# Kernel optimization log

Hardware: AMD Instinct MI355X
Metric: run time of the kernel (lower is better)

Reference implementation:

```python
import jax, jax.numpy as jnp
import numpy as np

D = 256
H = 4
DH = D // H
DFF = 1024
EPS = 1e-5


def _split_heads(x):
    B, L, _ = x.shape
    return x.reshape(B, L, H, DH).transpose(0, 2, 1, 3)  # [B,H,L,dh]


def _merge_heads(o):
    B, h, L, dh = o.shape
    return o.transpose(0, 2, 1, 3).reshape(B, L, h * dh)


def _attention(Q, K, V, M):
    # Q,K,V: [B,H,Lq/Lk,dh]; M: [B,Lq,Lk] or [B,1,Lk]
    A = jnp.einsum('bhqd,bhkd->bhqk', Q, K) / (DH ** 0.5)
    A = jnp.where(M[:, None] == 0, -jnp.inf, A)
    A = jax.nn.softmax(A, axis=-1)
    return jnp.einsum('bhqk,bhkd->bhqd', A, V)


def _layernorm(x, g, b):
    mu = jnp.mean(x, axis=-1, keepdims=True)
    var = jnp.mean(jnp.square(x - mu), axis=-1, keepdims=True)
    return (x - mu) * jax.lax.rsqrt(var + EPS) * g + b


def setup_inputs() -> dict:
    key = jax.random.key(0)
    ks = jax.random.split(key, 14)
    B, T, S = 16, 1024, 1024
    s = 1.0 / (D ** 0.5)
    inp = {
        'X_target': jax.random.normal(ks[0], (B, T, D), jnp.float32),
        'outputMask': jnp.ones((B, T), jnp.float32),
        'X_encoder': jax.random.normal(ks[1], (B, S, D), jnp.float32),
        'inputMask': jnp.ones((B, S), jnp.float32),
        'Wq1': jax.random.normal(ks[2], (D, D), jnp.float32) * s,
        'Wk1': jax.random.normal(ks[3], (D, D), jnp.float32) * s,
        'Wv1': jax.random.normal(ks[4], (D, D), jnp.float32) * s,
        'Wo1': jax.random.normal(ks[5], (D, D), jnp.float32) * s,
        'Wq2': jax.random.normal(ks[6], (D, D), jnp.float32) * s,
        'Wk2': jax.random.normal(ks[7], (D, D), jnp.float32) * s,
        'Wv2': jax.random.normal(ks[8], (D, D), jnp.float32) * s,
        'Wo2': jax.random.normal(ks[9], (D, D), jnp.float32) * s,
        'W1': jax.random.normal(ks[10], (DFF, D), jnp.float32) * s,
        'W2': jax.random.normal(ks[11], (D, DFF), jnp.float32) * (1.0 / (DFF ** 0.5)),
        'g1': jnp.ones((D,), jnp.float32), 'b1': jnp.zeros((D,), jnp.float32),
        'g2': jnp.ones((D,), jnp.float32), 'b2': jnp.zeros((D,), jnp.float32),
        'g3': jnp.ones((D,), jnp.float32), 'b3': jnp.zeros((D,), jnp.float32),
    }
    return inp


def reference(X_target, outputMask, X_encoder, inputMask,
              Wq1, Wk1, Wv1, Wo1, Wq2, Wk2, Wv2, Wo2,
              W1, W2, g1, b1, g2, b2, g3, b3):
    T = X_target.shape[1]
    # combined causal * padding mask (intended tril of ones)
    tril = jnp.tril(jnp.ones((T, T), X_target.dtype))
    M_self = outputMask[:, None, :] * tril  # [B,T,T]
    M_cross = inputMask[:, None, :]         # [B,1,S]

    # masked self-attention (Linear: x @ W.T)
    Q = _split_heads(X_target @ Wq1.T)
    K = _split_heads(X_target @ Wk1.T)
    V = _split_heads(X_target @ Wv1.T)
    O = _merge_heads(_attention(Q, K, V, M_self)) @ Wo1.T
    X = X_target + _layernorm(O, g1, b1)  # AddNorm (dropout eval=identity)

    # cross-attention; note: output proj is O @ Wo2 (no transpose) in source
    Q = _split_heads(X @ Wq2.T)
    K = _split_heads(X_encoder @ Wk2.T)
    V = _split_heads(X_encoder @ Wv2.T)
    O = _merge_heads(_attention(Q, K, V, M_cross)) @ Wo2
    X = X + _layernorm(O, g2, b2)

    # FFN with ReLU after both linears (as in source)
    F = jax.nn.relu(jax.nn.relu(X @ W1.T) @ W2.T)
    X = X + _layernorm(F, g3, b3)
    return X
```

## Files before the change

### kernel.cpp

```cpp
#include <hip/hip_runtime.h>
#include <math.h>

#define D_ 256
#define H_ 4
#define DH_ 64
#define NKT_ 16
#define TPB_BITS 10
#define SCL2E_ 0.18033688011112042f

typedef __attribute__((ext_vector_type(8))) short bf16x8;
typedef __attribute__((ext_vector_type(4))) short short4v;
typedef __attribute__((ext_vector_type(4))) float f32x4;

__device__ __forceinline__ short f2bf(float x) {
  union { float f; unsigned u; } c; c.f = x;
  unsigned r = (c.u + 0x7fffu + ((c.u >> 16) & 1u)) >> 16;
  return (short)r;
}
__device__ __forceinline__ float bf2f(short s) {
  union { unsigned u; float f; } c; c.u = ((unsigned)(unsigned short)s) << 16;
  return c.f;
}
__device__ __forceinline__ unsigned cvtpk(float lo, float hi) {
  unsigned r;
  asm("v_cvt_pk_bf16_f32 %0, %1, %2" : "=v"(r) : "v"(lo), "v"(hi));
  return r;
}
#if __has_builtin(__builtin_amdgcn_exp2f)
#define EXP2F(x) __builtin_amdgcn_exp2f(x)
#else
#define EXP2F(x) __expf(0.6931471805599453f * (x))
#endif

__device__ __forceinline__ void gl_lds16(const void* g, void* lds) {
  __builtin_amdgcn_global_load_lds((const __attribute__((address_space(1))) void*)g,
                                   (__attribute__((address_space(3))) void*)lds,
                                   16, 0, 0);
}

__global__ __launch_bounds__(256) void mask_bias(const float* __restrict__ m0,
                                                 const float* __restrict__ m1,
                                                 float* __restrict__ o0,
                                                 float* __restrict__ o1,
                                                 float* __restrict__ f0,
                                                 float* __restrict__ f1, int n) {
  int i = blockIdx.x * 256 + threadIdx.x;
  if (i < n) {
    o0[i] = (m0[i] != 0.f) ? 0.f : -1e30f;
    o1[i] = (m1[i] != 0.f) ? 0.f : -1e30f;
  }
  if (blockIdx.x == 0) {
    int t = threadIdx.x;
    const float* ms = m0 + (t >> 4) * 1024 + (t & 15) * 64;
    const float* mc = m1 + (t >> 4) * 1024 + (t & 15) * 64;
    float fs = 0.f, fc = 0.f;
    for (int j = 0; j < 64; ++j) {
      if (ms[j] == 0.f) fs = 1.f;
      if (mc[j] == 0.f) fc = 1.f;
    }
    f0[t] = fs; f1[t] = fc;
  }
}

template<int BN, bool ABF16, bool TRANSB, bool RELU, bool CBF16>
__global__ __launch_bounds__(256) void gemm_mfma(
    const void* __restrict__ A0, const void* __restrict__ A1, const void* __restrict__ A2,
    const float* __restrict__ B0, const float* __restrict__ B1, const float* __restrict__ B2,
    void* __restrict__ C0, void* __restrict__ C1, void* __restrict__ C2,
    int N, int K, int M, int vtrans_z, int ktile_z, int abf16_z, int qscale_z) {
  __shared__ short Al[2][128][72];
  __shared__ short Bl[2][BN][72];
  const int tid = threadIdx.x;
  const int w   = tid >> 6;
  const int l   = tid & 63;
  const int bn  = blockIdx.x * 128;
  const int bm  = blockIdx.y * BN;
  const int z   = blockIdx.z;
  const void*  Av = (z == 0) ? A0 : ((z == 1) ? A1 : A2);
  const float* B  = (z == 0) ? B0 : ((z == 1) ? B1 : B2);
  void*        Cv = (z == 0) ? C0 : ((z == 1) ? C1 : C2);
  const bool abf = ABF16 || (z == abf16_z);
  constexpr int NI = BN / 32;
  const int wm = (w >> 1) * 64;
  const int wn = (w & 1) * (BN / 2);
  const int fr = l & 15;
  const int fg = l >> 4;

  f32x4 acc[4][NI];
  #pragma unroll
  for (int mi = 0; mi < 4; ++mi)
    #pragma unroll
    for (int ni = 0; ni < NI; ++ni) acc[mi][ni] = (f32x4){0.f, 0.f, 0.f, 0.f};

  const int sr = tid >> 1;
  const int sc = (tid & 1) * 32;
  constexpr int BRF = (BN == 128) ? 8 : 4;
  const int brT = (BN == 128) ? (tid >> 1) : (tid >> 2);
  const int bcT = (BN == 128) ? ((tid & 1) * 32) : ((tid & 3) * 16);

  float4 arf[8]; bf16x8 arb[4]; float4 brf[8];

  auto loadA = [&](int k0) {
    if (abf) {
      const short* arow = (const short*)Av + (size_t)(bn + sr) * K + k0 + sc;
      #pragma unroll
      for (int i = 0; i < 4; ++i) arb[i] = *(const bf16x8*)&arow[i * 8];
    } else {
      const float* arow = (const float*)Av + (size_t)(bn + sr) * K + k0 + sc;
      #pragma unroll
      for (int i = 0; i < 8; ++i) arf[i] = *(const float4*)&arow[i * 4];
    }
  };
  auto loadB = [&](int k0) {
    if (TRANSB) {
      const float* brow = B + (size_t)(bm + brT) * K + k0 + bcT;
      #pragma unroll
      for (int i = 0; i < BRF; ++i) brf[i] = *(const float4*)&brow[i * 4];
    } else {
      #pragma unroll
      for (int i = 0; i < BRF; ++i) {
        int idx = tid + i * 256;
        int kk = (BN == 128) ? (idx >> 5) : (idx >> 4);
        int c4 = (BN == 128) ? ((idx & 31) * 4) : ((idx & 15) * 4);
        brf[i] = *(const float4*)&B[(size_t)(k0 + kk) * M + bm + c4];
      }
    }
  };
  auto store = [&](int buf) {
    if (abf) {
      #pragma unroll
      for (int i = 0; i < 4; ++i) *(bf16x8*)&Al[buf][sr][sc + i * 8] = arb[i];
    } else {
      #pragma unroll
      for (int i = 0; i < 8; ++i) {
        float4 v = arf[i];
        short4v s; s[0] = f2bf(v.x); s[1] = f2bf(v.y); s[2] = f2bf(v.z); s[3] = f2bf(v.w);
        *(short4v*)&Al[buf][sr][sc + i * 4] = s;
      }
    }
    if (TRANSB) {
      #pragma unroll
      for (int i = 0; i < BRF; ++i) {
        float4 v = brf[i];
        short4v s; s[0] = f2bf(v.x); s[1] = f2bf(v.y); s[2] = f2bf(v.z); s[3] = f2bf(v.w);
        *(short4v*)&Bl[buf][brT][bcT + i * 4] = s;
      }
    } else {
      #pragma unroll
      for (int i = 0; i < BRF; ++i) {
        int idx = tid + i * 256;
        int kk = (BN == 128) ? (idx >> 5) : (idx >> 4);
        int c4 = (BN == 128) ? ((idx & 31) * 4) : ((idx & 15) * 4);
        float4 v = brf[i];
        Bl[buf][c4 + 0][kk] = f2bf(v.x);
        Bl[buf][c4 + 1][kk] = f2bf(v.y);
        Bl[buf][c4 + 2][kk] = f2bf(v.z);
        Bl[buf][c4 + 3][kk] = f2bf(v.w);
      }
    }
  };

  loadA(0); loadB(0); store(0);
  __syncthreads();
  const int nk = K >> 6;
  for (int s = 0; s < nk; ++s) {
    const int cur = s & 1;
    if (s + 1 < nk) { loadA((s + 1) << 6); loadB((s + 1) << 6); }
    #pragma unroll
    for (int kh = 0; kh < 2; ++kh) {
      bf16x8 af[4], bfr[NI];
      #pragma unroll
      for (int mi = 0; mi < 4; ++mi)
        af[mi] = *(bf16x8*)&Al[cur][wm + mi * 16 + fr][kh * 32 + fg * 8];
      #pragma unroll
      for (int ni = 0; ni < NI; ++ni)
        bfr[ni] = *(bf16x8*)&Bl[cur][wn + ni * 16 + fr][kh * 32 + fg * 8];
      #pragma unroll
      for (int mi = 0; mi < 4; ++mi)
        #pragma unroll
        for (int ni = 0; ni < NI; ++ni)
          acc[mi][ni] = __builtin_amdgcn_mfma_f32_16x16x32_bf16(af[mi], bfr[ni], acc[mi][ni], 0, 0, 0);
    }
    if (s + 1 < nk) store(cur ^ 1);
    __syncthreads();
  }

  bool done = false;
  if constexpr (BN == 128) {
    if (z == vtrans_z) {
      done = true;
      #pragma unroll
      for (int mi = 0; mi < 4; ++mi) {
        int nbase = bn + wm + mi * 16 + fg * 4;
        int b_  = nbase >> TPB_BITS;
        int key = nbase & ((1 << TPB_BITS) - 1);
        int kt  = key >> 6, kin = key & 63;
        #pragma unroll
        for (int ni = 0; ni < 4; ++ni) {
          int col = bm + wn + ni * 16 + fr;
          int h_ = col >> 6, dh = col & 63;
          short4v s;
          #pragma unroll
          for (int reg = 0; reg < 4; ++reg) s[reg] = f2bf(acc[mi][ni][reg]);
          size_t off = ((((size_t)(b_ * H_ + h_) * NKT_) + kt) << 12)
                     + dh * 64 + (((kin >> 3) ^ (dh & 7)) << 3) + (kin & 7);
          *(short4v*)&((short*)Cv)[off] = s;
        }
      }
    } else if (z == ktile_z) {
      done = true;
      #pragma unroll
      for (int mi = 0; mi < 4; ++mi) {
        #pragma unroll
        for (int reg = 0; reg < 4; ++reg) {
          int tok = bn + wm + mi * 16 + fg * 4 + reg;
          int b_  = tok >> TPB_BITS;
          int key = tok & ((1 << TPB_BITS) - 1);
          int kt  = key >> 6, kin = key & 63;
          int fk  = (kin & 3) | (((kin >> 3) & 1) << 2);
          size_t tb = ((((size_t)(b_ * H_) * NKT_) + kt) << 12) + kin * 64;
          #pragma unroll
          for (int ni = 0; ni < 4; ++ni) {
            int col = bm + wn + ni * 16 + fr;
            int h_ = col >> 6, dh = col & 63;
            size_t off = tb + (((size_t)h_ * NKT_) << 12)
                       + (((dh >> 3) ^ fk) << 3) + (dh & 7);
            ((short*)Cv)[off] = f2bf(acc[mi][ni][reg]);
          }
        }
      }
    }
  }
  if (!done) {
    const float cs = (z == qscale_z) ? SCL2E_ : 1.f;
    #pragma unroll
    for (int mi = 0; mi < 4; ++mi) {
      #pragma unroll
      for (int reg = 0; reg < 4; ++reg) {
        size_t rowbase = (size_t)(bn + wm + mi * 16 + fg * 4 + reg) * M + bm + wn;
        #pragma unroll
        for (int ni = 0; ni < NI; ++ni) {
          float v = acc[mi][ni][reg] * cs;
          if (RELU) v = fmaxf(v, 0.f);
          if (CBF16) ((short*)Cv)[rowbase + ni * 16 + fr] = f2bf(v);
          else       ((float*)Cv)[rowbase + ni * 16 + fr] = v;
        }
      }
    }
  }
}

template<bool CAUSAL>
__global__ __launch_bounds__(256) void attn_mfma(const short* __restrict__ Q,
                                                 const short* __restrict__ KT,
                                                 const short* __restrict__ VT,
                                                 const float* __restrict__ bias,
                                                 const float* __restrict__ flags,
                                                 short* __restrict__ O,
                                                 int T, int Lk) {
  __shared__ short Kl[2][64][64];
  __shared__ short Vl[2][64][64];
  const int tid = threadIdx.x;
  const int l   = tid & 63;
  const int w   = tid >> 6;
  const int bh  = blockIdx.x;
  const int b   = bh >> 2;
  const int h   = bh & 3;
  const int r   = l & 15;
  const int g   = l >> 4;

  const short* Ktile = KT + (((size_t)bh * (Lk >> 6)) << 12);
  const short* Vtile = VT + (((size_t)bh * (Lk >> 6)) << 12);
  const float* brow  = bias + (size_t)b * Lk;
  const float* bfl   = flags + b * NKT_;

  const int qt  = CAUSAL ? ((T >> 6) - 1 - (int)blockIdx.y) : (int)blockIdx.y;
  const int nkt = CAUSAL ? (qt + 1) : (Lk >> 6);

  bf16x8 qf[2];
  {
    const short* qrow = Q + ((size_t)(b * T + qt * 64 + w * 16 + r)) * D_ + h * DH_;
    qf[0] = *(const bf16x8*)&qrow[g * 8];
    qf[1] = *(const bf16x8*)&qrow[32 + g * 8];
  }

  float m = -1e30f, ls = 0.f;
  f32x4 acc[4];
  #pragma unroll
  for (int dt = 0; dt < 4; ++dt) acc[dt] = (f32x4){0.f, 0.f, 0.f, 0.f};

  auto stage = [&](int kt, int bb) {
    const short* ks = Ktile + ((size_t)kt << 12) + w * 1024 + (size_t)l * 8;
    const short* vs = Vtile + ((size_t)kt << 12) + w * 1024 + (size_t)l * 8;
    char* kd = (char*)&Kl[bb][0][0] + w * 2048;
    char* vd = (char*)&Vl[bb][0][0] + w * 2048;
    gl_lds16(ks,       kd);
    gl_lds16(ks + 512, kd + 1024);
    gl_lds16(vs,       vd);
    gl_lds16(vs + 512, vd + 1024);
  };

  stage(0, 0);
  __syncthreads();

  const int rx = r & 7;
  const int rowp = 8 * (r >> 2) + (r & 3);
  for (int kt = 0; kt < nkt; ++kt) {
    const int buf = kt & 1;
    if (kt + 1 < nkt) stage(kt + 1, buf ^ 1);

    const char* kb = (const char*)&Kl[buf][0][0];
    const char* vb = (const char*)&Vl[buf][0][0];

    f32x4 sfr[4];
    #pragma unroll
    for (int st = 0; st < 4; ++st) sfr[st] = (f32x4){0.f, 0.f, 0.f, 0.f};
    __builtin_amdgcn_s_setprio(1);
    #pragma unroll
    for (int st = 0; st < 4; ++st) {
      const int rowk = 32 * (st >> 1) + 4 * (st & 1) + rowp;
      #pragma unroll
      for (int kh = 0; kh < 2; ++kh) {
        bf16x8 kf = *(const bf16x8*)(kb + rowk * 128 + (((kh * 4 + g) ^ rx) << 4));
        sfr[st] = __builtin_amdgcn_mfma_f32_16x16x32_bf16(kf, qf[kh], sfr[st], 0, 0, 0);
      }
    }
    __builtin_amdgcn_s_setprio(0);

    float sc[4][4];
    if (bfl[kt] != 0.f) {
      #pragma unroll
      for (int st = 0; st < 4; ++st) {
        float4 mv = *(const float4*)&brow[kt * 64 + 32 * (st >> 1) + 4 * (st & 1) + 8 * g];
        sc[st][0] = sfr[st][0] + mv.x;
        sc[st][1] = sfr[st][1] + mv.y;
        sc[st][2] = sfr[st][2] + mv.z;
        sc[st][3] = sfr[st][3] + mv.w;
      }
    } else {
      #pragma unroll
      for (int st = 0; st < 4; ++st)
        #pragma unroll
        for (int reg = 0; reg < 4; ++reg) sc[st][reg] = sfr[st][reg];
    }
    if (CAUSAL && kt == qt) {
      #pragma unroll
      for (int st = 0; st < 4; ++st)
        #pragma unroll
        for (int reg = 0; reg < 4; ++reg)
          if (32 * (st >> 1) + 4 * (st & 1) + 8 * g + reg > w * 16 + r)
            sc[st][reg] = -1e30f;
    }

    float t0 = fmaxf(fmaxf(sc[0][0], sc[0][1]), sc[0][2]);
    float t1 = fmaxf(fmaxf(sc[0][3], sc[1][0]), sc[1][1]);
    float t2 = fmaxf(fmaxf(sc[1][2], sc[1][3]), sc[2][0]);
    float t3 = fmaxf(fmaxf(sc[2][1], sc[2][2]), sc[2][3]);
    float t4 = fmaxf(fmaxf(sc[3][0], sc[3][1]), sc[3][2]);
    float tm = fmaxf(fmaxf(fmaxf(t0, t1), fmaxf(t2, t3)), fmaxf(t4, sc[3][3]));
    tm = fmaxf(tm, __shfl_xor(tm, 16));
    tm = fmaxf(tm, __shfl_xor(tm, 32));
    const int need = __any(tm - m > 8.f);
    float mnew = need ? fmaxf(m, tm) : m;
    float pe[4][4], psum = 0.f;
    #pragma unroll
    for (int st = 0; st < 4; ++st)
      #pragma unroll
      for (int reg = 0; reg < 4; ++reg) {
        pe[st][reg] = EXP2F(sc[st][reg] - mnew);
        psum += pe[st][reg];
      }
    psum += __shfl_xor(psum, 16);
    psum += __shfl_xor(psum, 32);

    union { unsigned u[4]; bf16x8 v; } pa, pb;
    pa.u[0] = cvtpk(pe[0][0], pe[0][1]);
    pa.u[1] = cvtpk(pe[0][2], pe[0][3]);
    pa.u[2] = cvtpk(pe[1][0], pe[1][1]);
    pa.u[3] = cvtpk(pe[1][2], pe[1][3]);
    pb.u[0] = cvtpk(pe[2][0], pe[2][1]);
    pb.u[1] = cvtpk(pe[2][2], pe[2][3]);
    pb.u[2] = cvtpk(pe[3][0], pe[3][1]);
    pb.u[3] = cvtpk(pe[3][2], pe[3][3]);

    if (need) {
      float alpha = EXP2F(m - mnew);
      ls = ls * alpha + psum;
      m = mnew;
      float af[4];
      #pragma unroll
      for (int reg = 0; reg < 4; ++reg) af[reg] = __shfl(alpha, g * 4 + reg);
      #pragma unroll
      for (int dt = 0; dt < 4; ++dt)
        #pragma unroll
        for (int reg = 0; reg < 4; ++reg) acc[dt][reg] *= af[reg];
    } else {
      ls += psum;
    }

    __builtin_amdgcn_s_setprio(1);
    #pragma unroll
    for (int kh = 0; kh < 2; ++kh) {
      bf16x8 pf = (kh == 0) ? pa.v : pb.v;
      #pragma unroll
      for (int dt = 0; dt < 4; ++dt) {
        bf16x8 vf = *(const bf16x8*)(vb + (dt * 16 + r) * 128 + (((kh * 4 + g) ^ rx) << 4));
        acc[dt] = __builtin_amdgcn_mfma_f32_16x16x32_bf16(pf, vf, acc[dt], 0, 0, 0);
      }
    }
    __builtin_amdgcn_s_setprio(0);

    __syncthreads();
  }

  float inv = (ls > 0.f) ? (1.f / ls) : 0.f;
  float invf[4];
  #pragma unroll
  for (int reg = 0; reg < 4; ++reg) invf[reg] = __shfl(inv, g * 4 + reg);
  #pragma unroll
  for (int reg = 0; reg < 4; ++reg) {
    short* orow = O + ((size_t)(b * T + qt * 64 + w * 16 + g * 4 + reg)) * D_ + h * DH_;
    #pragma unroll
    for (int dt = 0; dt < 4; ++dt)
      orow[dt * 16 + r] = f2bf(acc[dt][reg] * invf[reg]);
  }
}

template<bool RBF16, bool OBF16>
__global__ __launch_bounds__(256) void ln_res(const short* __restrict__ F,
                                              const void* __restrict__ Rv,
                                              const float* __restrict__ g,
                                              const float* __restrict__ bt,
                                              void* __restrict__ outv) {
  const int lane = threadIdx.x & 63;
  const int wid  = threadIdx.x >> 6;
  const size_t row  = (size_t)blockIdx.x * 4 + wid;
  const size_t base = row * 256 + (size_t)lane * 4;
  short4v fv = *(const short4v*)&F[base];
  float vx = bf2f(fv[0]), vy = bf2f(fv[1]), vz = bf2f(fv[2]), vw = bf2f(fv[3]);
  float s = vx + vy + vz + vw;
  #pragma unroll
  for (int o = 32; o >= 1; o >>= 1) s += __shfl_xor(s, o);
  float mu = s * (1.f / 256.f);
  float dx = vx - mu, dy = vy - mu, dz = vz - mu, dw = vw - mu;
  float vr = dx * dx + dy * dy + dz * dz + dw * dw;
  #pragma unroll
  for (int o = 32; o >= 1; o >>= 1) vr += __shfl_xor(vr, o);
  float rstd = rsqrtf(vr * (1.f / 256.f) + 1e-5f);
  float4 g4 = *(const float4*)&g[lane * 4];
  float4 b4 = *(const float4*)&bt[lane * 4];
  float rx, ry, rz, rw;
  if (RBF16) {
    short4v r4 = *(const short4v*)&((const short*)Rv)[base];
    rx = bf2f(r4[0]); ry = bf2f(r4[1]); rz = bf2f(r4[2]); rw = bf2f(r4[3]);
  } else {
    float4 r4 = *(const float4*)&((const float*)Rv)[base];
    rx = r4.x; ry = r4.y; rz = r4.z; rw = r4.w;
  }
  float ox = fmaf(dx * rstd, g4.x, b4.x) + rx;
  float oy = fmaf(dy * rstd, g4.y, b4.y) + ry;
  float oz = fmaf(dz * rstd, g4.z, b4.z) + rz;
  float ow = fmaf(dw * rstd, g4.w, b4.w) + rw;
  if (OBF16) {
    uint2 u; u.x = cvtpk(ox, oy); u.y = cvtpk(oz, ow);
    *(uint2*)&((short*)outv)[base] = u;
  } else {
    *(float4*)&((float*)outv)[base] = make_float4(ox, oy, oz, ow);
  }
}

extern "C" void kernel_launch(void* const* d_in, const int* in_sizes, int n_in,
                              void* d_out, int out_size, void* d_ws, size_t ws_size,
                              hipStream_t stream) {
  const float* Xt    = (const float*)d_in[0];
  const float* oMask = (const float*)d_in[1];
  const float* Xe    = (const float*)d_in[2];
  const float* iMask = (const float*)d_in[3];
  const float* Wq1   = (const float*)d_in[4];
  const float* Wk1   = (const float*)d_in[5];
  const float* Wv1   = (const float*)d_in[6];
  const float* Wo1   = (const float*)d_in[7];
  const float* Wq2   = (const float*)d_in[8];
  const float* Wk2   = (const float*)d_in[9];
  const float* Wv2   = (const float*)d_in[10];
  const float* Wo2   = (const float*)d_in[11];
  const float* W1    = (const float*)d_in[12];
  const float* W2    = (const float*)d_in[13];
  const float* g1    = (const float*)d_in[14];
  const float* b1    = (const float*)d_in[15];
  const float* g2    = (const float*)d_in[16];
  const float* b2    = (const float*)d_in[17];
  const float* g3    = (const float*)d_in[18];
  const float* b3    = (const float*)d_in[19];

  const int B = 16, T = 1024, S = 1024;
  const int NT = B * T;
  const size_t SZ = (size_t)NT * 256;

  float* ws = (float*)d_ws;
  float* s0 = ws;
  float* s1 = ws + SZ;
  float* s2 = ws + 2 * SZ;
  float* s3 = ws + 3 * SZ;
  float* s4 = ws + 4 * SZ;
  float* s5 = ws + 5 * SZ;
  short* b_s0 = (short*)s0; short* b_s1 = (short*)s1; short* b_s2 = (short*)s2;
  short* b_s3 = (short*)s3; short* b_s4 = (short*)s4; short* b_s5 = (short*)s5;
  float* biasS = s3 + 3 * (SZ / 4);
  float* biasC = biasS + B * S;
  float* flagS = biasC + B * S;
  float* flagC = flagS + B * NKT_;

  dim3 blk(256);
  dim3 gQKV(NT / 128, 2, 3);
  dim3 gS64(NT / 128, 4, 1);
  dim3 gF1(NT / 128, 8, 1);
  dim3 gA(B * H_, T / 64);

  mask_bias<<<64, blk, 0, stream>>>(oMask, iMask, biasS, biasC, flagS, flagC, B * T);

  gemm_mfma<128, false, true, false, true><<<gQKV, blk, 0, stream>>>(
      Xt, Xt, Xt, Wq1, Wk1, Wv1, s0, s1, s2, NT, 256, 256, 2, 1, -1, 0);
  attn_mfma<true><<<gA, blk, 0, stream>>>(b_s0, b_s1, b_s2, biasS, flagS, b_s3, T, T);
  gemm_mfma<64, true, true, false, true><<<gS64, blk, 0, stream>>>(
      s3, s3, s3, Wo1, Wo1, Wo1, s0, s0, s0, NT, 256, 256, -1, -1, -1, -1);
  ln_res<false, true><<<NT / 4, blk, 0, stream>>>(b_s0, Xt, g1, b1, b_s4);

  gemm_mfma<128, false, true, false, true><<<gQKV, blk, 0, stream>>>(
      s4, Xe, Xe, Wq2, Wk2, Wv2, s0, s1, s2, NT, 256, 256, 2, 1, 0, 0);
  attn_mfma<false><<<gA, blk, 0, stream>>>(b_s0, b_s1, b_s2, biasC, flagC, b_s3, T, S);
  gemm_mfma<64, true, false, false, true><<<gS64, blk, 0, stream>>>(
      s3, s3, s3, Wo2, Wo2, Wo2, s0, s0, s0, NT, 256, 256, -1, -1, -1, -1);
  ln_res<true, true><<<NT / 4, blk, 0, stream>>>(b_s0, b_s4, g2, b2, b_s5);

  gemm_mfma<128, true, true, true, true><<<gF1, blk, 0, stream>>>(
      s5, s5, s5, W1, W1, W1, s0, s0, s0, NT, 256, 1024, -1, -1, -1, -1);
  gemm_mfma<64, true, true, true, true><<<gS64, blk, 0, stream>>>(
      s0, s0, s0, W2, W2, W2, s4, s4, s4, NT, 1024, 256, -1, -1, -1, -1);
  ln_res<true, false><<<NT / 4, blk, 0, stream>>>(b_s4, b_s5, g3, b3, (float*)d_out);
}
```

Measured before the change: 210.3 us.

## Use packed bf16 converts, reorder causal tiles, tree-reduce softmax row sum

```diff
diff --git a/kernel.cpp b/kernel.cpp
--- a/kernel.cpp
+++ b/kernel.cpp
@@ -25,6 +25,9 @@
   unsigned r;
   asm("v_cvt_pk_bf16_f32 %0, %1, %2" : "=v"(r) : "v"(lo), "v"(hi));
   return r;
+}
+__device__ __forceinline__ uint2 cvtpk4(float4 v) {
+  uint2 u; u.x = cvtpk(v.x, v.y); u.y = cvtpk(v.z, v.w); return u;
 }
 #if __has_builtin(__builtin_amdgcn_exp2f)
 #define EXP2F(x) __builtin_amdgcn_exp2f(x)
@@ -132,19 +135,13 @@
       for (int i = 0; i < 4; ++i) *(bf16x8*)&Al[buf][sr][sc + i * 8] = arb[i];
     } else {
       #pragma unroll
-      for (int i = 0; i < 8; ++i) {
-        float4 v = arf[i];
-        short4v s; s[0] = f2bf(v.x); s[1] = f2bf(v.y); s[2] = f2bf(v.z); s[3] = f2bf(v.w);
-        *(short4v*)&Al[buf][sr][sc + i * 4] = s;
-      }
+      for (int i = 0; i < 8; ++i)
+        *(uint2*)&Al[buf][sr][sc + i * 4] = cvtpk4(arf[i]);
     }
     if (TRANSB) {
       #pragma unroll
-      for (int i = 0; i < BRF; ++i) {
-        float4 v = brf[i];
-        short4v s; s[0] = f2bf(v.x); s[1] = f2bf(v.y); s[2] = f2bf(v.z); s[3] = f2bf(v.w);
-        *(short4v*)&Bl[buf][brT][bcT + i * 4] = s;
-      }
+      for (int i = 0; i < BRF; ++i)
+        *(uint2*)&Bl[buf][brT][bcT + i * 4] = cvtpk4(brf[i]);
     } else {
       #pragma unroll
       for (int i = 0; i < BRF; ++i) {
@@ -199,12 +196,12 @@
         for (int ni = 0; ni < 4; ++ni) {
           int col = bm + wn + ni * 16 + fr;
           int h_ = col >> 6, dh = col & 63;
-          short4v s;
-          #pragma unroll
-          for (int reg = 0; reg < 4; ++reg) s[reg] = f2bf(acc[mi][ni][reg]);
+          uint2 u;
+          u.x = cvtpk(acc[mi][ni][0], acc[mi][ni][1]);
+          u.y = cvtpk(acc[mi][ni][2], acc[mi][ni][3]);
           size_t off = ((((size_t)(b_ * H_ + h_) * NKT_) + kt) << 12)
                      + dh * 64 + (((kin >> 3) ^ (dh & 7)) << 3) + (kin & 7);
-          *(short4v*)&((short*)Cv)[off] = s;
+          *(uint2*)&((short*)Cv)[off] = u;
         }
       }
     } else if (z == ktile_z) {
@@ -274,7 +271,8 @@
   const float* brow  = bias + (size_t)b * Lk;
   const float* bfl   = flags + b * NKT_;
 
-  const int qt  = CAUSAL ? ((T >> 6) - 1 - (int)blockIdx.y) : (int)blockIdx.y;
+  const int by  = (int)blockIdx.y;
+  const int qt  = CAUSAL ? (by < 8 ? 15 - by : by - 8) : by;
   const int nkt = CAUSAL ? (qt + 1) : (Lk >> 6);
 
   bf16x8 qf[2];
@@ -362,14 +360,17 @@
     tm = fmaxf(tm, __shfl_xor(tm, 32));
     const int need = __any(tm - m > 8.f);
     float mnew = need ? fmaxf(m, tm) : m;
-    float pe[4][4], psum = 0.f;
+    float pe[4][4];
     #pragma unroll
     for (int st = 0; st < 4; ++st)
       #pragma unroll
-      for (int reg = 0; reg < 4; ++reg) {
+      for (int reg = 0; reg < 4; ++reg)
         pe[st][reg] = EXP2F(sc[st][reg] - mnew);
-        psum += pe[st][reg];
-      }
+    float ps0 = (pe[0][0] + pe[0][1]) + (pe[0][2] + pe[0][3]);
+    float ps1 = (pe[1][0] + pe[1][1]) + (pe[1][2] + pe[1][3]);
+    float ps2 = (pe[2][0] + pe[2][1]) + (pe[2][2] + pe[2][3]);
+    float ps3 = (pe[3][0] + pe[3][1]) + (pe[3][2] + pe[3][3]);
+    float psum = (ps0 + ps1) + (ps2 + ps3);
     psum += __shfl_xor(psum, 16);
     psum += __shfl_xor(psum, 32);
 
```

Measured after the change: 213.4 us. No clear change (+1.5%).
